# Optimization experiments

Hardware: AMD Instinct MI355X
Metric: run time of the kernel (lower is better)

The kernel has to match this reference:

```python
import math
import jax, jax.numpy as jnp
import numpy as np

# ---- static config (matches init_kwargs) ----
B, L, D = 32, 1024, 256
H = 4
E = D // H          # head dim = 64
LF = L // 2 + 1     # rfft bins = 513
LEFT, RIGHT = 205, 513   # retained freq band: int(LF*(1-0.6)) .. LF  (i=0, global mixer)
SPATIAL_RATIO = 0.1
TOP_K = int(5 * math.log(L))  # factor=5 -> 34
LN_EPS = 1e-8


def _layer_norm(x, g, b):
    m = jnp.mean(x, axis=-1, keepdims=True)
    v = jnp.mean((x - m) ** 2, axis=-1, keepdims=True)
    return (x - m) / jnp.sqrt(v + LN_EPS) * g + b


def _gelu_erf(x):
    return x * 0.5 * (1.0 + jax.lax.erf(x / math.sqrt(2.0)))


def _time_delay_agg_training(values, corr):
    # values, corr: [B,H,E,L]; shared top-k delay indices across batch (training path)
    mean_value = jnp.mean(corr, axis=(1, 2))                  # [B,L]
    _, index = jax.lax.top_k(jnp.mean(mean_value, axis=0), TOP_K)  # [TOP_K] int32
    weights = mean_value[:, index]                            # [B,TOP_K]
    tmp_corr = jax.nn.softmax(weights, axis=-1)               # [B,TOP_K]
    t = jnp.arange(L)

    def body(acc, args):
        idx, w = args                                         # idx: scalar delay, w: [B]
        pattern = jnp.take(values, (t + idx) % L, axis=-1)    # roll(values, -idx, axis=-1)
        return acc + pattern * w[:, None, None, None], None

    acc, _ = jax.lax.scan(body, jnp.zeros_like(values), (index, tmp_corr.T))
    return acc                                                # [B,H,E,L]


def setup_inputs() -> dict:
    key = jax.random.key(0)
    ks = jax.random.split(key, 12)
    lin = lambda k: jax.random.normal(k, (D, D), jnp.float32) * 0.02  # stored [in,out]
    return {
        "x": jax.random.normal(ks[0], (B, L, D), jnp.float32),
        "Wq": lin(ks[1]), "bq": jnp.zeros((D,), jnp.float32),
        "Wk": lin(ks[2]), "bk": jnp.zeros((D,), jnp.float32),
        "Wv": lin(ks[3]), "bv": jnp.zeros((D,), jnp.float32),
        "Wd": lin(ks[4]), "bd": jnp.zeros((D,), jnp.float32),
        "ln1_g": jnp.ones((D,), jnp.float32), "ln1_b": jnp.zeros((D,), jnp.float32),
        "W1": lin(ks[5]), "b1": jnp.zeros((D,), jnp.float32),
        "W2": lin(ks[6]), "b2": jnp.zeros((D,), jnp.float32),
        "ln2_g": jnp.ones((D,), jnp.float32), "ln2_b": jnp.zeros((D,), jnp.float32),
    }


def reference(x, Wq, bq, Wk, bk, Wv, bv, Wd, bd, ln1_g, ln1_b, W1, b1, W2, b2, ln2_g, ln2_b):
    # ---- HybridAttention ----
    q = (x @ Wq + bq).reshape(B, L, H, E).transpose(0, 2, 3, 1)  # [B,H,E,L]
    k = (x @ Wk + bk).reshape(B, L, H, E).transpose(0, 2, 3, 1)
    v = (x @ Wv + bv).reshape(B, L, H, E).transpose(0, 2, 3, 1)

    q_fft = jnp.fft.rfft(q, axis=-1)      # [B,H,E,LF]
    k_fft = jnp.fft.rfft(k, axis=-1)
    mask = jnp.zeros((LF,), jnp.float32).at[LEFT:RIGHT].set(1.0)

    # band-limited autocorrelation (equivalent to the index-box scatter/gather)
    corr = jnp.fft.irfft(q_fft * jnp.conj(k_fft) * mask, n=L, axis=-1)  # [B,H,E,L]
    Vt = _time_delay_agg_training(v, corr)                              # [B,H,E,L]
    context_time = Vt.transpose(0, 3, 1, 2).reshape(B, L, D)

    # spatial (band-pass filtered) attention branch
    v_fft = jnp.fft.rfft(v, axis=-1)
    qs = jnp.fft.irfft(q_fft * mask, n=L, axis=-1).transpose(0, 1, 3, 2)  # [B,H,L,E]
    ks_ = jnp.fft.irfft(k_fft * mask, n=L, axis=-1).transpose(0, 1, 3, 2)
    vs = jnp.fft.irfft(v_fft * mask, n=L, axis=-1).transpose(0, 1, 3, 2)
    scores = jnp.einsum('bhle,bhse->bhls', qs, ks_) / math.sqrt(E)
    probs = jax.nn.softmax(scores, axis=-1)
    ctx_sp = jnp.einsum('bhls,bhse->bhle', probs, vs).transpose(0, 2, 1, 3).reshape(B, L, D)

    context = (1.0 - SPATIAL_RATIO) * context_time + SPATIAL_RATIO * ctx_sp
    h = _layer_norm(context @ Wd + bd + x, ln1_g, ln1_b)

    # ---- FeedForward ----
    f = _gelu_erf(h @ W1 + b1) @ W2 + b2
    return _layer_norm(f + h, ln2_g, ln2_b)
```

## Files before the change

### kernel.cpp

```cpp
#include <hip/hip_runtime.h>
#include <hip/hip_bf16.h>
#include <math.h>

#define Lc 1024
#define Dc 256
#define Bc 32
#define Hc 4
#define Ec 64
#define TOPK 34
#define LEFTc 205

typedef unsigned short u16;
typedef __attribute__((ext_vector_type(8))) short bf16x8;
typedef __attribute__((ext_vector_type(4))) float f32x4;

__device__ __forceinline__ float bf2f(u16 u) {
    return __uint_as_float(((unsigned)u) << 16);
}
__device__ __forceinline__ u16 f2bf(float f) {
    unsigned u = __float_as_uint(f);
    u += 0x7FFFu + ((u >> 16) & 1u);
    return (u16)(u >> 16);
}

__global__ void detect_k(const u16* __restrict__ x, int* __restrict__ flag) {
    __shared__ int cnt;
    if (threadIdx.x == 0) cnt = 0;
    __syncthreads();
    int bad = 0;
    for (int i = threadIdx.x; i < 4096; i += 256) {
        float a = fabsf(bf2f(x[i]));
        if (!(a == 0.0f || (a >= 1e-8f && a <= 1e8f))) bad++;
    }
    atomicAdd(&cnt, bad);
    __syncthreads();
    if (threadIdx.x == 0) *flag = (cnt > 512) ? 1 : 0;
}

struct SrcPtrs { const void* p[17]; };
__global__ __launch_bounds__(256) void ingest_all_k(
    SrcPtrs sp, u16* __restrict__ cx, u16* __restrict__ wts, const int* __restrict__ flag)
{
    const long NB = (long)Bc * Lc * Dc;
    long i = (long)blockIdx.x * 256 + threadIdx.x;
    const int fp = *flag;
    const void* src; u16* dst; long off;
    if (i < NB) {
        src = sp.p[0]; dst = cx; off = i;
    } else {
        long j = i - NB;
        if (j < 6L * 65536) {
            const int w = (int)(j >> 16); off = j & 65535;
            const int wsidx[6] = {1, 3, 5, 7, 11, 13};
            src = sp.p[wsidx[w]]; dst = wts + (long)w * 65536;
        } else {
            long k2 = j - 6L * 65536;
            if (k2 >= 2560) return;
            const int v = (int)(k2 >> 8); off = k2 & 255;
            const int vsidx[10] = {2, 4, 6, 8, 9, 10, 12, 14, 15, 16};
            src = sp.p[vsidx[v]]; dst = wts + 6L * 65536 + (long)v * 256;
        }
    }
    dst[off] = fp ? f2bf(((const float*)src)[off]) : ((const u16*)src)[off];
}

__global__ void build_h(float* __restrict__ hf) {
    int d = blockIdx.x * blockDim.x + threadIdx.x;
    if (d >= Lc) return;
    float s = 0.f;
    for (int f = LEFTc; f < 512; ++f) {
        int m = (f * d) & (Lc - 1);
        s += __cosf((float)m * 6.135923151542565e-3f);
    }
    float ny = (d & 1) ? -1.f : 1.f;
    hf[d] = (2.f * s + ny) * (1.f / 1024.f);
}

__global__ void build_G(const float* __restrict__ hf, u16* __restrict__ G) {
    int i = blockIdx.x * 256 + threadIdx.x;
    int t = i >> 10, s = i & (Lc - 1);
    G[i] = f2bf(hf[(t - s) & (Lc - 1)]);
}

__global__ __launch_bounds__(256) void transpose_k(
    const u16* __restrict__ in, u16* __restrict__ out)
{
    __shared__ u16 t[32][33];
    const int l0 = blockIdx.x * 32, d0 = blockIdx.y * 32, b = blockIdx.z;
    const int tx = threadIdx.x & 31, ty = threadIdx.x >> 5;
    const u16* ib = in + (size_t)b * Lc * Dc;
    #pragma unroll
    for (int i = 0; i < 4; ++i)
        t[ty + i * 8][tx] = ib[(size_t)(l0 + ty + i * 8) * Dc + d0 + tx];
    __syncthreads();
    u16* ob = out + (size_t)b * Dc * Lc;
    #pragma unroll
    for (int i = 0; i < 4; ++i)
        ob[(size_t)(d0 + ty + i * 8) * Lc + l0 + tx] = t[tx][ty + i * 8];
}

__global__ __launch_bounds__(256) void wtrans_k(
    const u16* __restrict__ src, u16* __restrict__ dst)
{
    __shared__ u16 t[32][33];
    const int c0 = blockIdx.x * 32, r0 = blockIdx.y * 32;
    const u16* s = src + (size_t)blockIdx.z * 65536;
    u16* d = dst + (size_t)blockIdx.z * 65536;
    const int tx = threadIdx.x & 31, ty = threadIdx.x >> 5;
    #pragma unroll
    for (int i = 0; i < 4; ++i)
        t[ty + i * 8][tx] = s[(r0 + ty + i * 8) * 256 + c0 + tx];
    __syncthreads();
    #pragma unroll
    for (int i = 0; i < 4; ++i)
        d[(c0 + ty + i * 8) * 256 + r0 + tx] = t[tx][ty + i * 8];
}

template <int EPI, bool ACOMB>
__global__ __launch_bounds__(256) void mgemm_k(
    const u16* __restrict__ Abase, const u16* __restrict__ A2base,
    const u16* __restrict__ BTbase, const u16* __restrict__ bias,
    const u16* __restrict__ resid, u16* __restrict__ Cbase,
    int M, int N, int K, long strA, long strBT, long strC)
{
    const int z = blockIdx.z;
    const u16* A  = Abase + (size_t)z * strA;
    const u16* BT = BTbase + (size_t)z * strBT;
    u16* C        = Cbase + (size_t)z * strC;
    const int tid = threadIdx.x;
    const int wave = tid >> 6, lane = tid & 63;
    const int m16 = lane & 15, quad = lane >> 4;
    const int m0 = blockIdx.y * 128 + wave * 32;
    const int n0 = blockIdx.x * 64;

    __shared__ __align__(16) u16 sB[8192];

    const u16* arow0 = A + (size_t)(m0 + m16) * K + quad * 8;
    const u16* arow1 = arow0 + (size_t)16 * K;
    const u16* a2row0 = ACOMB ? (A2base + (size_t)z * strA + (size_t)(m0 + m16) * K + quad * 8) : nullptr;
    const u16* a2row1 = ACOMB ? (a2row0 + (size_t)16 * K) : nullptr;

    f32x4 acc[2][4] = {};

    #pragma unroll 1
    for (int kc = 0; kc < K; kc += 128) {
        __syncthreads();
        #pragma unroll
        for (int i = 0; i < 4; ++i) {
            const int c = tid + i * 256;
            const int nr = c >> 4, ko = c & 15;
            const bf16x8 v = *(const bf16x8*)(BT + (size_t)(n0 + nr) * K + kc + ko * 8);
            *(bf16x8*)(sB + ((nr >> 4) * 4 + (ko >> 2)) * 512 + (ko & 3) * 128
                          + (((nr & 15) ^ (ko & 3))) * 8) = v;
        }
        __syncthreads();
        #pragma unroll
        for (int kf = 0; kf < 4; ++kf) {
            bf16x8 a0 = *(const bf16x8*)(arow0 + kc + kf * 32);
            bf16x8 a1 = *(const bf16x8*)(arow1 + kc + kf * 32);
            if (ACOMB) {
                const bf16x8 x0 = *(const bf16x8*)(a2row0 + kc + kf * 32);
                const bf16x8 x1 = *(const bf16x8*)(a2row1 + kc + kf * 32);
                #pragma unroll
                for (int j = 0; j < 8; ++j) {
                    a0[j] = (short)f2bf(0.9f * bf2f((u16)a0[j]) + 0.1f * bf2f((u16)x0[j]));
                    a1[j] = (short)f2bf(0.9f * bf2f((u16)a1[j]) + 0.1f * bf2f((u16)x1[j]));
                }
            }
            #pragma unroll
            for (int nt = 0; nt < 4; ++nt) {
                const bf16x8 bf = *(const bf16x8*)(sB + (nt * 4 + kf) * 512 + quad * 128
                                                      + ((m16 ^ quad)) * 8);
                acc[0][nt] = __builtin_amdgcn_mfma_f32_16x16x32_bf16(a0, bf, acc[0][nt], 0, 0, 0);
                acc[1][nt] = __builtin_amdgcn_mfma_f32_16x16x32_bf16(a1, bf, acc[1][nt], 0, 0, 0);
            }
        }
    }

    #pragma unroll
    for (int ms = 0; ms < 2; ++ms) {
        #pragma unroll
        for (int nt = 0; nt < 4; ++nt) {
            const int col = n0 + nt * 16 + m16;
            const float bv = bias ? bf2f(bias[col]) : 0.f;
            #pragma unroll
            for (int r = 0; r < 4; ++r) {
                const size_t off = (size_t)(m0 + ms * 16 + quad * 4 + r) * N + col;
                float v = acc[ms][nt][r] + bv;
                if (EPI == 1) v += bf2f(resid[off]);
                if (EPI == 2) v = 0.5f * v * (1.0f + erff(v * 0.70710678118654752f));
                C[off] = f2bf(v);
            }
        }
    }
}

__global__ __launch_bounds__(256) void corr_k(
    const u16* __restrict__ qs, const u16* __restrict__ ks, float* __restrict__ mv)
{
    const int l = blockIdx.x;
    const int b = ((l & 7) << 2) | ((l >> 3) & 3);
    const int rest = l >> 5;
    const int g = rest & 15;
    const int uq = rest >> 4;
    const int wave = threadIdx.x >> 6, lane = threadIdx.x & 63;
    const int m16 = lane & 15, quad = lane >> 4;
    const size_t base = (size_t)b * Lc * Dc;

    __shared__ float red[4][124];
    for (int i = threadIdx.x; i < 4 * 124; i += 256) ((float*)red)[i] = 0.f;
    __syncthreads();

    f32x4 acc[4] = {};
    #pragma unroll
    for (int ui = 0; ui < 4; ++ui) {
        const int u = uq * 16 + wave * 4 + ui;
        const u16* qrow = qs + base + (size_t)(u * 16 + m16) * Dc + quad * 8;
        const u16* kr[4];
        #pragma unroll
        for (int al = 0; al < 4; ++al) {
            const int s = (u - g * 4 - al) & 63;
            kr[al] = ks + base + (size_t)(s * 16 + m16) * Dc + quad * 8;
        }
        #pragma unroll
        for (int k0 = 0; k0 < Dc; k0 += 32) {
            const bf16x8 aq = *(const bf16x8*)(qrow + k0);
            #pragma unroll
            for (int al = 0; al < 4; ++al) {
                const bf16x8 bk = *(const bf16x8*)(kr[al] + k0);
                acc[al] = __builtin_amdgcn_mfma_f32_16x16x32_bf16(aq, bk, acc[al], 0, 0, 0);
            }
        }
    }

    #pragma unroll
    for (int al = 0; al < 4; ++al)
        #pragma unroll
        for (int r = 0; r < 4; ++r)
            atomicAdd(&red[wave][al * 31 + quad * 4 + r - m16 + 15], acc[al][r]);
    __syncthreads();

    if (threadIdx.x < 124) {
        const int al = threadIdx.x / 31, dd = threadIdx.x % 31;
        const float s = red[0][threadIdx.x] + red[1][threadIdx.x] +
                        red[2][threadIdx.x] + red[3][threadIdx.x];
        atomicAdd(&mv[b * Lc + (((g * 4 + al) * 16 + dd - 15) & (Lc - 1))], s);
    }
}

__global__ __launch_bounds__(256) void attn_k(
    const u16* __restrict__ qs, const u16* __restrict__ ks,
    const u16* __restrict__ vsT, u16* __restrict__ ctx)
{
    const int lt = blockIdx.x, h = blockIdx.y, b = blockIdx.z;

    __shared__ __align__(16) u16 sK[8192];
    __shared__ __align__(16) u16 sV[8192];
    __shared__ __align__(16) u16 sP[8192];

    const int tid  = threadIdx.x;
    const int wave = tid >> 6;
    const int lane = tid & 63;
    const int m16  = lane & 15;
    const int quad = lane >> 4;
    const int l0   = lt * 64;
    const size_t base = (size_t)b * Lc * Dc + (size_t)h * Ec;
    const size_t vtbase = ((size_t)b * Dc + (size_t)h * Ec) * Lc;

    const u16* qrow = qs + base + (size_t)(l0 + wave * 16 + m16) * Dc + quad * 8;
    const bf16x8 qa0 = *(const bf16x8*)(qrow);
    const bf16x8 qa1 = *(const bf16x8*)(qrow + 32);

    f32x4 o[4] = {};
    float rs[4] = {0.f, 0.f, 0.f, 0.f};

    const int rsw = m16 ^ quad;

    #pragma unroll 1
    for (int s0 = 0; s0 < Lc; s0 += 128) {
        __syncthreads();
        #pragma unroll
        for (int i = 0; i < 4; ++i) {
            const int c = tid + i * 256;
            {
                const int sr = c >> 3, eo = c & 7;
                const bf16x8 v = *(const bf16x8*)(ks + base + (size_t)(s0 + sr) * Dc + eo * 8);
                *(bf16x8*)(sK + ((sr >> 4) * 2 + (eo >> 2)) * 512 + (eo & 3) * 128
                              + (((sr & 15) ^ (eo & 3))) * 8) = v;
            }
            {
                const int er = c >> 4, so = c & 15;
                const bf16x8 v = *(const bf16x8*)(vsT + vtbase + (size_t)er * Lc + s0 + so * 8);
                *(bf16x8*)(sV + ((er >> 4) * 4 + (so >> 2)) * 512 + (so & 3) * 128
                              + (((er & 15) ^ (so & 3))) * 8) = v;
            }
        }
        __syncthreads();

        #pragma unroll
        for (int st = 0; st < 8; ++st) {
            const bf16x8 kb0 = *(const bf16x8*)(sK + (st * 2 + 0) * 512 + quad * 128 + rsw * 8);
            const bf16x8 kb1 = *(const bf16x8*)(sK + (st * 2 + 1) * 512 + quad * 128 + rsw * 8);
            f32x4 c4 = {0.f, 0.f, 0.f, 0.f};
            c4 = __builtin_amdgcn_mfma_f32_16x16x32_bf16(qa0, kb0, c4, 0, 0, 0);
            c4 = __builtin_amdgcn_mfma_f32_16x16x32_bf16(qa1, kb1, c4, 0, 0, 0);
            const int q2 = ((st & 1) << 1) | (m16 >> 3);
            u16* pw = sP + wave * 2048 + (st >> 1) * 512 + q2 * 128 + (m16 & 7);
            #pragma unroll
            for (int r = 0; r < 4; ++r) {
                const float p = __expf(c4[r] * 0.125f);
                rs[r] += p;
                pw[(quad * 4 + r) * 8] = f2bf(p);
            }
        }
        __syncthreads();

        const bf16x8 a0 = *(const bf16x8*)(sP + wave * 2048 + 0 * 512 + quad * 128 + m16 * 8);
        const bf16x8 a1 = *(const bf16x8*)(sP + wave * 2048 + 1 * 512 + quad * 128 + m16 * 8);
        const bf16x8 a2 = *(const bf16x8*)(sP + wave * 2048 + 2 * 512 + quad * 128 + m16 * 8);
        const bf16x8 a3 = *(const bf16x8*)(sP + wave * 2048 + 3 * 512 + quad * 128 + m16 * 8);
        #pragma unroll
        for (int nt = 0; nt < 4; ++nt) {
            o[nt] = __builtin_amdgcn_mfma_f32_16x16x32_bf16(a0, *(const bf16x8*)(sV + (nt * 4 + 0) * 512 + quad * 128 + rsw * 8), o[nt], 0, 0, 0);
            o[nt] = __builtin_amdgcn_mfma_f32_16x16x32_bf16(a1, *(const bf16x8*)(sV + (nt * 4 + 1) * 512 + quad * 128 + rsw * 8), o[nt], 0, 0, 0);
            o[nt] = __builtin_amdgcn_mfma_f32_16x16x32_bf16(a2, *(const bf16x8*)(sV + (nt * 4 + 2) * 512 + quad * 128 + rsw * 8), o[nt], 0, 0, 0);
            o[nt] = __builtin_amdgcn_mfma_f32_16x16x32_bf16(a3, *(const bf16x8*)(sV + (nt * 4 + 3) * 512 + quad * 128 + rsw * 8), o[nt], 0, 0, 0);
        }
    }

    #pragma unroll
    for (int off = 1; off < 16; off <<= 1) {
        #pragma unroll
        for (int r = 0; r < 4; ++r) rs[r] += __shfl_xor(rs[r], off);
    }
    #pragma unroll
    for (int nt = 0; nt < 4; ++nt) {
        #pragma unroll
        for (int r = 0; r < 4; ++r)
            ctx[base + (size_t)(l0 + wave * 16 + quad * 4 + r) * Dc + nt * 16 + m16] =
                f2bf(o[nt][r] / rs[r]);
    }
}

__global__ __launch_bounds__(1024) void topk_k(
    const float* __restrict__ mv, int* __restrict__ idx_g, float* __restrict__ w_g)
{
    __shared__ float wvs[16];
    __shared__ int   wis[16];
    __shared__ int   widx;
    __shared__ int   sidx[TOPK];
    const int tid = threadIdx.x;
    const int lane = tid & 63;
    const int wv_id = tid >> 6;

    float g = 0.f;
    for (int b = 0; b < Bc; ++b) g += mv[b * Lc + tid];

    for (int j = 0; j < TOPK; ++j) {
        float v = g; int ix = tid;
        #pragma unroll
        for (int off = 32; off > 0; off >>= 1) {
            const float ov = __shfl_xor(v, off);
            const int   oi = __shfl_xor(ix, off);
            if (ov > v || (ov == v && oi < ix)) { v = ov; ix = oi; }
        }
        if (lane == 0) { wvs[wv_id] = v; wis[wv_id] = ix; }
        __syncthreads();
        if (tid == 0) {
            float bv = wvs[0]; int bi = wis[0];
            for (int u = 1; u < 16; ++u)
                if (wvs[u] > bv || (wvs[u] == bv && wis[u] < bi)) { bv = wvs[u]; bi = wis[u]; }
            widx = bi; sidx[j] = bi; idx_g[j] = bi;
        }
        __syncthreads();
        if (tid == widx) g = -3e38f;
        __syncthreads();
    }
    if (tid < Bc) {
        float wv[TOPK];
        float mx = -3e38f;
        for (int j = 0; j < TOPK; ++j) {
            wv[j] = mv[tid * Lc + sidx[j]] * (1.0f / (float)Dc);
            mx = fmaxf(mx, wv[j]);
        }
        float sum = 0.f;
        for (int j = 0; j < TOPK; ++j) { wv[j] = expf(wv[j] - mx); sum += wv[j]; }
        for (int j = 0; j < TOPK; ++j) w_g[tid * TOPK + j] = wv[j] / sum;
    }
}

__global__ __launch_bounds__(256) void agg_k(
    const u16* __restrict__ v, const int* __restrict__ idx,
    const float* __restrict__ w, u16* __restrict__ ct)
{
    const int b = blockIdx.y;
    const int t = blockIdx.x * 4 + (threadIdx.x >> 6);
    const int lane = threadIdx.x & 63;
    __shared__ int   sidx[TOPK];
    __shared__ float sw[TOPK];
    if (threadIdx.x < TOPK) { sidx[threadIdx.x] = idx[threadIdx.x]; sw[threadIdx.x] = w[b * TOPK + threadIdx.x]; }
    __syncthreads();
    const u16* vb = v + (size_t)b * Lc * Dc;
    const int c4 = lane * 4;
    float a0 = 0.f, a1 = 0.f, a2 = 0.f, a3 = 0.f;
    for (int j = 0; j < TOPK; ++j) {
        const float wj = sw[j];
        const ushort4 u = *reinterpret_cast<const ushort4*>(
            vb + (size_t)((t + sidx[j]) & (Lc - 1)) * Dc + c4);
        a0 += wj * bf2f(u.x); a1 += wj * bf2f(u.y);
        a2 += wj * bf2f(u.z); a3 += wj * bf2f(u.w);
    }
    ushort4 o; o.x = f2bf(a0); o.y = f2bf(a1); o.z = f2bf(a2); o.w = f2bf(a3);
    *reinterpret_cast<ushort4*>(ct + (size_t)b * Lc * Dc + (size_t)t * Dc + c4) = o;
}

template <bool FINAL>
__global__ __launch_bounds__(256) void ln_k(
    const u16* __restrict__ in, const u16* __restrict__ g,
    const u16* __restrict__ be, void* __restrict__ out, const int* __restrict__ flag)
{
    const int wave = threadIdx.x >> 6, lane = threadIdx.x & 63;
    const int row = blockIdx.x * 4 + wave;
    const int c4 = lane * 4;
    const ushort4 u = *reinterpret_cast<const ushort4*>(in + (size_t)row * Dc + c4);
    float x[4] = {bf2f(u.x), bf2f(u.y), bf2f(u.z), bf2f(u.w)};
    float sm = x[0] + x[1] + x[2] + x[3];
    float sq = x[0]*x[0] + x[1]*x[1] + x[2]*x[2] + x[3]*x[3];
    #pragma unroll
    for (int off = 1; off < 64; off <<= 1) {
        sm += __shfl_xor(sm, off);
        sq += __shfl_xor(sq, off);
    }
    const float mean = sm * (1.f / 256.f);
    const float var = sq * (1.f / 256.f) - mean * mean;
    const float rstd = __frsqrt_rn(var + 1e-8f);
    const ushort4 gg = *reinterpret_cast<const ushort4*>(g + c4);
    const ushort4 bb = *reinterpret_cast<const ushort4*>(be + c4);
    float y[4];
    y[0] = (x[0] - mean) * rstd * bf2f(gg.x) + bf2f(bb.x);
    y[1] = (x[1] - mean) * rstd * bf2f(gg.y) + bf2f(bb.y);
    y[2] = (x[2] - mean) * rstd * bf2f(gg.z) + bf2f(bb.z);
    y[3] = (x[3] - mean) * rstd * bf2f(gg.w) + bf2f(bb.w);
    if (FINAL && *flag) {
        float4 o = make_float4(y[0], y[1], y[2], y[3]);
        *reinterpret_cast<float4*>((float*)out + (size_t)row * Dc + c4) = o;
    } else {
        ushort4 o; o.x = f2bf(y[0]); o.y = f2bf(y[1]); o.z = f2bf(y[2]); o.w = f2bf(y[3]);
        *reinterpret_cast<ushort4*>((u16*)out + (size_t)row * Dc + c4) = o;
    }
}

extern "C" void kernel_launch(void* const* d_in, const int* in_sizes, int n_in,
                              void* d_out, int out_size, void* d_ws, size_t ws_size,
                              hipStream_t stream)
{
    (void)in_sizes; (void)n_in; (void)out_size; (void)ws_size;

    const size_t BLD = (size_t)Bc * Lc * Dc;
    const size_t SLOT = BLD * 2;
    const long LD = (long)(Lc * Dc);
    char* ws = (char*)d_ws;
    u16* b0 = (u16*)(ws + 0 * SLOT);
    u16* b1 = (u16*)(ws + 1 * SLOT);
    u16* b2 = (u16*)(ws + 2 * SLOT);
    u16* b3 = (u16*)(ws + 3 * SLOT);
    u16* cx = (u16*)(ws + 4 * SLOT);
    u16* G  = (u16*)(ws + 5 * SLOT);
    char* tail = ws + 5 * SLOT + (size_t)Lc * Lc * 2;
    u16* wts  = (u16*)tail;
    u16* wtsT = wts + 6 * 65536 + 10 * 256;
    char* tail2 = (char*)(wtsT + 6 * 65536);
    float* hf  = (float*)(tail2 + 512);
    float* mv  = hf + Lc;
    int*   idx = (int*)(mv + Bc * Lc);
    float* wsm = (float*)(idx + 64);
    int*   flag = (int*)(wsm + Bc * TOPK);

    u16* vecs = wts + 6 * 65536;
    u16* cbv = vecs + 2 * 256;  u16* cbd = vecs + 3 * 256;
    u16* l1g = vecs + 4 * 256;  u16* l1b = vecs + 5 * 256;
    u16* cb1 = vecs + 6 * 256;  u16* cb2 = vecs + 7 * 256;
    u16* l2g = vecs + 8 * 256;  u16* l2b = vecs + 9 * 256;
    u16* wvT = wtsT + 2 * 65536;
    u16* wdT = wtsT + 3 * 65536; u16* w1T = wtsT + 4 * 65536; u16* w2T = wtsT + 5 * 65536;

    detect_k<<<dim3(1), 256, 0, stream>>>((const u16*)d_in[0], flag);
    SrcPtrs sp;
    for (int i = 0; i < 17; ++i) sp.p[i] = d_in[i];
    ingest_all_k<<<dim3(34314), 256, 0, stream>>>(sp, cx, wts, flag);
    wtrans_k<<<dim3(8, 8, 6), 256, 0, stream>>>(wts, wtsT);

    build_h<<<dim3(4), 256, 0, stream>>>(hf);
    build_G<<<dim3((Lc * Lc) / 256), 256, 0, stream>>>(hf, G);

    transpose_k<<<dim3(32, 8, 32), 256, 0, stream>>>(cx, b1);
    mgemm_k<0, false><<<dim3(4, 8, 32), 256, 0, stream>>>(
        G, nullptr, b1, nullptr, nullptr, b0, Lc, Dc, Lc, 0, LD, LD);

    mgemm_k<0, false><<<dim3(4, 256, 3), 256, 0, stream>>>(
        b0, nullptr, wtsT, nullptr, nullptr, b1, Bc * Lc, Dc, Dc, 0, 65536, (long)BLD);

    hipMemsetAsync(mv, 0, (size_t)Bc * Lc * 4, stream);
    corr_k<<<dim3(2048), 256, 0, stream>>>(b1, b2, mv);

    transpose_k<<<dim3(32, 8, 32), 256, 0, stream>>>(b3, b0);
    attn_k<<<dim3(16, 4, 32), 256, 0, stream>>>(b1, b2, b0, b3);

    topk_k<<<dim3(1), 1024, 0, stream>>>(mv, idx, wsm);

    const dim3 gProj(4, 256, 1);
    mgemm_k<0, false><<<gProj, 256, 0, stream>>>(cx, nullptr, wvT, cbv, nullptr, b1, Bc * Lc, Dc, Dc, 0, 0, 0);
    agg_k<<<dim3(256, 32), 256, 0, stream>>>(b1, idx, wsm, b2);

    mgemm_k<1, true><<<gProj, 256, 0, stream>>>(b2, b3, wdT, cbd, cx, b0, Bc * Lc, Dc, Dc, 0, 0, 0);

    ln_k<false><<<dim3(8192), 256, 0, stream>>>(b0, l1g, l1b, b1, flag);

    mgemm_k<2, false><<<gProj, 256, 0, stream>>>(b1, nullptr, w1T, cb1, nullptr, b2, Bc * Lc, Dc, Dc, 0, 0, 0);
    mgemm_k<1, false><<<gProj, 256, 0, stream>>>(b2, nullptr, w2T, cb2, b1, b3, Bc * Lc, Dc, Dc, 0, 0, 0);

    ln_k<true><<<dim3(8192), 256, 0, stream>>>(b3, l2g, l2b, d_out, flag);
}
```

Measured before the change: 654.5 us.

## Register-prefetch next K/V and B tiles; swizzle P tile in LDS

In both the GEMM and spatial-attention kernels, the next global tile is loaded into registers while the current LDS tile is consumed, so global load latency overlaps with MFMA work. The barrier structure moves to a store-sync-compute-sync pattern. The attention kernel also XOR-swizzles P-tile writes and reads in LDS to cut bank conflicts. This costs extra registers for the prefetch buffers, which could lower occupancy.

```diff
diff --git a/kernel.cpp b/kernel.cpp
--- a/kernel.cpp
+++ b/kernel.cpp
@@ -140,20 +140,32 @@
     const u16* a2row0 = ACOMB ? (A2base + (size_t)z * strA + (size_t)(m0 + m16) * K + quad * 8) : nullptr;
     const u16* a2row1 = ACOMB ? (a2row0 + (size_t)16 * K) : nullptr;
 
+    const u16* bgp[4];
+    u16* bls[4];
+    #pragma unroll
+    for (int i = 0; i < 4; ++i) {
+        const int c = tid + i * 256;
+        const int nr = c >> 4, ko = c & 15;
+        bgp[i] = BT + (size_t)(n0 + nr) * K + ko * 8;
+        bls[i] = sB + ((nr >> 4) * 4 + (ko >> 2)) * 512 + (ko & 3) * 128
+                    + (((nr & 15) ^ (ko & 3))) * 8;
+    }
+
+    bf16x8 breg[4];
+    #pragma unroll
+    for (int i = 0; i < 4; ++i) breg[i] = *(const bf16x8*)(bgp[i]);
+
     f32x4 acc[2][4] = {};
 
     #pragma unroll 1
     for (int kc = 0; kc < K; kc += 128) {
-        __syncthreads();
-        #pragma unroll
-        for (int i = 0; i < 4; ++i) {
-            const int c = tid + i * 256;
-            const int nr = c >> 4, ko = c & 15;
-            const bf16x8 v = *(const bf16x8*)(BT + (size_t)(n0 + nr) * K + kc + ko * 8);
-            *(bf16x8*)(sB + ((nr >> 4) * 4 + (ko >> 2)) * 512 + (ko & 3) * 128
-                          + (((nr & 15) ^ (ko & 3))) * 8) = v;
-        }
-        __syncthreads();
+        #pragma unroll
+        for (int i = 0; i < 4; ++i) *(bf16x8*)(bls[i]) = breg[i];
+        __syncthreads();
+        if (kc + 128 < K) {
+            #pragma unroll
+            for (int i = 0; i < 4; ++i) breg[i] = *(const bf16x8*)(bgp[i] + kc + 128);
+        }
         #pragma unroll
         for (int kf = 0; kf < 4; ++kf) {
             bf16x8 a0 = *(const bf16x8*)(arow0 + kc + kf * 32);
@@ -175,6 +187,7 @@
                 acc[1][nt] = __builtin_amdgcn_mfma_f32_16x16x32_bf16(a1, bf, acc[1][nt], 0, 0, 0);
             }
         }
+        __syncthreads();
     }
 
     #pragma unroll
@@ -271,31 +284,50 @@
     const bf16x8 qa0 = *(const bf16x8*)(qrow);
     const bf16x8 qa1 = *(const bf16x8*)(qrow + 32);
 
+    const u16* kgp[4]; const u16* vgp[4];
+    u16* kls[4]; u16* vls[4];
+    #pragma unroll
+    for (int i = 0; i < 4; ++i) {
+        const int c = tid + i * 256;
+        const int sr = c >> 3, eo = c & 7;
+        kgp[i] = ks + base + (size_t)sr * Dc + eo * 8;
+        kls[i] = sK + ((sr >> 4) * 2 + (eo >> 2)) * 512 + (eo & 3) * 128
+                    + (((sr & 15) ^ (eo & 3))) * 8;
+        const int er = c >> 4, so = c & 15;
+        vgp[i] = vsT + vtbase + (size_t)er * Lc + so * 8;
+        vls[i] = sV + ((er >> 4) * 4 + (so >> 2)) * 512 + (so & 3) * 128
+                    + (((er & 15) ^ (so & 3))) * 8;
+    }
+
+    bf16x8 kreg[4], vreg[4];
+    #pragma unroll
+    for (int i = 0; i < 4; ++i) {
+        kreg[i] = *(const bf16x8*)(kgp[i]);
+        vreg[i] = *(const bf16x8*)(vgp[i]);
+    }
+
     f32x4 o[4] = {};
     float rs[4] = {0.f, 0.f, 0.f, 0.f};
 
     const int rsw = m16 ^ quad;
+    const int hrd = ((quad & 1) << 1) | (m16 >> 3);
+    const int prd = (m16 ^ hrd) * 8;
 
     #pragma unroll 1
     for (int s0 = 0; s0 < Lc; s0 += 128) {
-        __syncthreads();
         #pragma unroll
         for (int i = 0; i < 4; ++i) {
-            const int c = tid + i * 256;
-            {
-                const int sr = c >> 3, eo = c & 7;
-                const bf16x8 v = *(const bf16x8*)(ks + base + (size_t)(s0 + sr) * Dc + eo * 8);
-                *(bf16x8*)(sK + ((sr >> 4) * 2 + (eo >> 2)) * 512 + (eo & 3) * 128
-                              + (((sr & 15) ^ (eo & 3))) * 8) = v;
+            *(bf16x8*)(kls[i]) = kreg[i];
+            *(bf16x8*)(vls[i]) = vreg[i];
+        }
+        __syncthreads();
+        if (s0 + 128 < Lc) {
+            #pragma unroll
+            for (int i = 0; i < 4; ++i) {
+                kreg[i] = *(const bf16x8*)(kgp[i] + (size_t)(s0 + 128) * Dc);
+                vreg[i] = *(const bf16x8*)(vgp[i] + (s0 + 128));
             }
-            {
-                const int er = c >> 4, so = c & 15;
-                const bf16x8 v = *(const bf16x8*)(vsT + vtbase + (size_t)er * Lc + s0 + so * 8);
-                *(bf16x8*)(sV + ((er >> 4) * 4 + (so >> 2)) * 512 + (so & 3) * 128
-                              + (((er & 15) ^ (so & 3))) * 8) = v;
-            }
-        }
-        __syncthreads();
+        }
 
         #pragma unroll
         for (int st = 0; st < 8; ++st) {
@@ -305,20 +337,21 @@
             c4 = __builtin_amdgcn_mfma_f32_16x16x32_bf16(qa0, kb0, c4, 0, 0, 0);
             c4 = __builtin_amdgcn_mfma_f32_16x16x32_bf16(qa1, kb1, c4, 0, 0, 0);
             const int q2 = ((st & 1) << 1) | (m16 >> 3);
+            const int hst = ((q2 & 1) << 1) | (quad >> 1);
             u16* pw = sP + wave * 2048 + (st >> 1) * 512 + q2 * 128 + (m16 & 7);
             #pragma unroll
             for (int r = 0; r < 4; ++r) {
                 const float p = __expf(c4[r] * 0.125f);
                 rs[r] += p;
-                pw[(quad * 4 + r) * 8] = f2bf(p);
+                pw[(((quad * 4 + r) ^ hst)) * 8] = f2bf(p);
             }
         }
         __syncthreads();
 
-        const bf16x8 a0 = *(const bf16x8*)(sP + wave * 2048 + 0 * 512 + quad * 128 + m16 * 8);
-        const bf16x8 a1 = *(const bf16x8*)(sP + wave * 2048 + 1 * 512 + quad * 128 + m16 * 8);
-        const bf16x8 a2 = *(const bf16x8*)(sP + wave * 2048 + 2 * 512 + quad * 128 + m16 * 8);
-        const bf16x8 a3 = *(const bf16x8*)(sP + wave * 2048 + 3 * 512 + quad * 128 + m16 * 8);
+        const bf16x8 a0 = *(const bf16x8*)(sP + wave * 2048 + 0 * 512 + quad * 128 + prd);
+        const bf16x8 a1 = *(const bf16x8*)(sP + wave * 2048 + 1 * 512 + quad * 128 + prd);
+        const bf16x8 a2 = *(const bf16x8*)(sP + wave * 2048 + 2 * 512 + quad * 128 + prd);
+        const bf16x8 a3 = *(const bf16x8*)(sP + wave * 2048 + 3 * 512 + quad * 128 + prd);
         #pragma unroll
         for (int nt = 0; nt < 4; ++nt) {
             o[nt] = __builtin_amdgcn_mfma_f32_16x16x32_bf16(a0, *(const bf16x8*)(sV + (nt * 4 + 0) * 512 + quad * 128 + rsw * 8), o[nt], 0, 0, 0);
@@ -326,6 +359,7 @@
             o[nt] = __builtin_amdgcn_mfma_f32_16x16x32_bf16(a2, *(const bf16x8*)(sV + (nt * 4 + 2) * 512 + quad * 128 + rsw * 8), o[nt], 0, 0, 0);
             o[nt] = __builtin_amdgcn_mfma_f32_16x16x32_bf16(a3, *(const bf16x8*)(sV + (nt * 4 + 3) * 512 + quad * 128 + rsw * 8), o[nt], 0, 0, 0);
         }
+        __syncthreads();
     }
 
     #pragma unroll
```

New measurement: 621.1 us. 5.1% less time.
